# Performance work log

Hardware: AMD Instinct MI355X
Metric: run time of the kernel (lower is better)

The kernel has to match this reference:

```python
import jax, jax.numpy as jnp
import numpy as np

N_LIT, N_CLAUSE, N_EDGES, D = 100000, 400000, 1200000, 128


def setup_inputs() -> dict:
    key = jax.random.key(0)
    ks = jax.random.split(key, 9)
    s = 1.0 / np.sqrt(D)  # PyTorch LSTM init: U(-1/sqrt(hidden), 1/sqrt(hidden))
    x_l = jax.random.normal(ks[0], (N_LIT, D), jnp.float32)
    h0 = jax.random.normal(ks[1], (N_CLAUSE, D), jnp.float32)
    c0 = jax.random.normal(ks[2], (N_CLAUSE, D), jnp.float32)
    W_ih = jax.random.uniform(ks[3], (4 * D, D), jnp.float32, -s, s)
    W_hh = jax.random.uniform(ks[4], (4 * D, D), jnp.float32, -s, s)
    b_ih = jax.random.uniform(ks[5], (4 * D,), jnp.float32, -s, s)
    b_hh = jax.random.uniform(ks[6], (4 * D,), jnp.float32, -s, s)
    edge_lit = jax.random.randint(ks[7], (N_EDGES,), 0, N_LIT, jnp.int32)
    edge_clause = jnp.sort(jax.random.randint(ks[8], (N_EDGES,), 0, N_CLAUSE, jnp.int32))
    return {"x_l": x_l, "h0": h0, "c0": c0, "W_ih": W_ih, "W_hh": W_hh,
            "b_ih": b_ih, "b_hh": b_hh, "edge_lit": edge_lit, "edge_clause": edge_clause}


def reference(x_l, h0, c0, W_ih, W_hh, b_ih, b_hh, edge_lit, edge_clause):
    n_clauses = h0.shape[0]
    # msg = adj_t @ x_l : sparse aggregation of literal features into clauses
    msg = jax.ops.segment_sum(x_l[edge_lit], edge_clause, num_segments=n_clauses)  # [n_clauses, D]
    # Single-timestep LSTM cell (seq_len=1, batch=n_clauses); PyTorch gate order i,f,g,o
    gates = msg @ W_ih.T + b_ih + h0 @ W_hh.T + b_hh  # [n_clauses, 4D]
    i, f, g, o = jnp.split(gates, 4, axis=-1)
    i = jax.nn.sigmoid(i)
    f = jax.nn.sigmoid(f)
    g = jnp.tanh(g)
    o = jax.nn.sigmoid(o)
    c_new = f * c0 + i * g
    h_new = o * jnp.tanh(c_new)
    return (h_new, c_new)
```

## Files before the change

### kernel.cpp

```cpp
#include <hip/hip_runtime.h>
#include <hip/hip_bf16.h>


using frag_ab = __attribute__((ext_vector_type(8))) short;
using frag_cd = __attribute__((ext_vector_type(4))) float;

__device__ __forceinline__ float bf2f(unsigned short u) {
    union { unsigned u; float f; } v; v.u = ((unsigned)u) << 16; return v.f;
}
__device__ __forceinline__ unsigned short f2bf(float f) {
    __hip_bfloat16 h = __float2bfloat16(f);
    return *reinterpret_cast<unsigned short*>(&h);
}
__device__ __forceinline__ float sigm(float x) {
    return __builtin_amdgcn_rcpf(1.0f + __builtin_amdgcn_exp2f(-1.442695040889f * x));
}
__device__ __forceinline__ float tanh_fast(float x) {
    float s = __builtin_amdgcn_rcpf(1.0f + __builtin_amdgcn_exp2f(-2.885390081777f * x));
    return __builtin_fmaf(2.0f, s, -1.0f);
}
__device__ __forceinline__ frag_ab load8_fp32(const float* p) {
    float4 a = *reinterpret_cast<const float4*>(p);
    float4 b = *reinterpret_cast<const float4*>(p + 4);
    frag_ab r;
    r[0] = (short)f2bf(a.x); r[1] = (short)f2bf(a.y);
    r[2] = (short)f2bf(a.z); r[3] = (short)f2bf(a.w);
    r[4] = (short)f2bf(b.x); r[5] = (short)f2bf(b.y);
    r[6] = (short)f2bf(b.z); r[7] = (short)f2bf(b.w);
    return r;
}

#define WS_BPACK_OFF  0
#define WS_BIAS_OFF   262144
#define WS_FLAG_OFF   264192
#define WS_ROWPTR_OFF 264704

#define EDGE_CAP 512

__global__ void detect_fmt(const unsigned short* __restrict__ x, int* __restrict__ flag) {
    int t = threadIdx.x;
    int cnt = 0;
    for (int i = t; i < 4096; i += 64) {
        unsigned e = (x[2 * i] >> 7) & 0xFF;
        cnt += (e >= 0xC0) ? 1 : 0;
    }
    #pragma unroll
    for (int s = 32; s; s >>= 1) cnt += __shfl_xor(cnt, s);
    if (t == 0) *flag = (cnt > 64) ? 1 : 0;
}

__global__ void build_rowptr(const int* __restrict__ edge_clause, int* __restrict__ rowptr,
                             int n_edges, int n_clause) {
    int idx = blockIdx.x * blockDim.x + threadIdx.x;
    if (idx > n_clause) return;
    int lo = 0, hi = n_edges;
    while (lo < hi) {
        int mid = (lo + hi) >> 1;
        if (edge_clause[mid] < idx) lo = mid + 1; else hi = mid;
    }
    rowptr[idx] = lo;
}

template <int FP32IN>
__global__ void prepack(const void* __restrict__ W_ih_, const void* __restrict__ W_hh_,
                        const void* __restrict__ b_ih_, const void* __restrict__ b_hh_,
                        unsigned short* __restrict__ Bpack, float* __restrict__ bias,
                        const int* __restrict__ flag) {
    if (*flag != FP32IN) return;
    int idx = blockIdx.x * blockDim.x + threadIdx.x;
    if (idx < 16384) {
        int kk = idx >> 11;
        int n  = (idx >> 2) & 511;
        int lq = idx & 3;
        int ksrc = (kk & 3) * 32 + lq * 8;
        frag_ab v;
        if constexpr (FP32IN) {
            const float* W = (kk < 4) ? (const float*)W_ih_ : (const float*)W_hh_;
            v = load8_fp32(W + (size_t)n * 128 + ksrc);
        } else {
            const unsigned short* W =
                (kk < 4) ? (const unsigned short*)W_ih_ : (const unsigned short*)W_hh_;
            v = *reinterpret_cast<const frag_ab*>(W + (size_t)n * 128 + ksrc);
        }
        *reinterpret_cast<frag_ab*>(Bpack + (size_t)idx * 8) = v;
    }
    if (idx < 512) {
        float b;
        if constexpr (FP32IN)
            b = ((const float*)b_ih_)[idx] + ((const float*)b_hh_)[idx];
        else
            b = bf2f(((const unsigned short*)b_ih_)[idx]) +
                bf2f(((const unsigned short*)b_hh_)[idx]);
        bias[idx] = b;
    }
}

template <int FP32IN>
__global__ __launch_bounds__(512, 4) void lit2clause_fused(
    const void* __restrict__ x_l_,
    const void* __restrict__ h0_,
    const void* __restrict__ c0_,
    const unsigned short* __restrict__ Bpack,
    const float* __restrict__ bias,
    const int*  __restrict__ rowptr_g,
    const int*  __restrict__ edge_lit,
    void* __restrict__ out_,
    const int* __restrict__ fmt_flag,
    int n_clause)
{
    if (*fmt_flag != FP32IN) return;

    __shared__ __align__(16) unsigned char SH[32768];
    __shared__ int elits[EDGE_CAP];
    unsigned char* Amsg = SH;
    unsigned char* Ah0  = SH + 16384;
    float* LDSf = (float*)SH;

    const int tid  = threadIdx.x;
    const int lane = tid & 63;
    const int w    = tid >> 6;
    const int cbase = blockIdx.x * 64;

    int rp_l = 0;
    if (lane < 9) rp_l = rowptr_g[cbase + w * 8 + lane];

    const int eBase = rowptr_g[cbase];
    const int eEnd  = rowptr_g[cbase + 64];
    const int eCount = eEnd - eBase;
    for (int i = tid; i < eCount && i < EDGE_CAP; i += 512)
        elits[i] = edge_lit[eBase + i];

    #pragma unroll
    for (int q0 = 0; q0 < 2; ++q0) {
        int q = tid + q0 * 512;
        int row = q >> 4;
        int j   = q & 15;
        frag_ab v;
        if constexpr (FP32IN) {
            v = load8_fp32((const float*)h0_ + (size_t)(cbase + row) * 128 + j * 8);
        } else {
            v = *reinterpret_cast<const frag_ab*>(
                (const unsigned short*)h0_ + (size_t)(cbase + row) * 128 + j * 8);
        }
        int byte = (j * 16) ^ ((row & 7) << 4);
        *reinterpret_cast<frag_ab*>(Ah0 + row * 256 + byte) = v;
    }
    __syncthreads();

    {
        const int q   = lane >> 4;
        const int l16 = lane & 15;
        for (int s = 0; s < 8; ++s) {
            int cc = w * 8 + s;
            int st = __shfl(rp_l, s)     - eBase;
            int en = __shfl(rp_l, s + 1) - eBase;
            float a[8] = {0.f, 0.f, 0.f, 0.f, 0.f, 0.f, 0.f, 0.f};
            for (int e = st + q; e < en; e += 4) {
                int lit = (e < EDGE_CAP) ? elits[e] : edge_lit[eBase + e];
                if constexpr (FP32IN) {
                    const float* xr = (const float*)x_l_ + (size_t)lit * 128 + l16 * 8;
                    float4 v0 = *reinterpret_cast<const float4*>(xr);
                    float4 v1 = *reinterpret_cast<const float4*>(xr + 4);
                    a[0] += v0.x; a[1] += v0.y; a[2] += v0.z; a[3] += v0.w;
                    a[4] += v1.x; a[5] += v1.y; a[6] += v1.z; a[7] += v1.w;
                } else {
                    const unsigned short* xr =
                        (const unsigned short*)x_l_ + (size_t)lit * 128 + l16 * 8;
                    frag_ab v = *reinterpret_cast<const frag_ab*>(xr);
                    #pragma unroll
                    for (int j = 0; j < 8; ++j) a[j] += bf2f((unsigned short)v[j]);
                }
            }
            #pragma unroll
            for (int j = 0; j < 8; ++j) {
                a[j] += __shfl_xor(a[j], 16);
                a[j] += __shfl_xor(a[j], 32);
            }
            if (q == 0) {
                frag_ab o;
                #pragma unroll
                for (int j = 0; j < 8; ++j) o[j] = (short)f2bf(a[j]);
                int byte = (l16 * 16) ^ ((cc & 7) << 4);
                *reinterpret_cast<frag_ab*>(Amsg + cc * 256 + byte) = o;
            }
        }
    }
    __syncthreads();

    const int l15 = lane & 15;
    const int lq  = lane >> 4;
    const int d = w * 16 + l15;

    float cold[4][4];
    #pragma unroll
    for (int mf = 0; mf < 4; ++mf) {
        #pragma unroll
        for (int r = 0; r < 4; ++r) {
            int m = cbase + mf * 16 + lq * 4 + r;
            if constexpr (FP32IN) cold[mf][r] = ((const float*)c0_)[(size_t)m * 128 + d];
            else cold[mf][r] = bf2f(((const unsigned short*)c0_)[(size_t)m * 128 + d]);
        }
    }

    frag_cd acc[4][4];
    #pragma unroll
    for (int g = 0; g < 4; ++g)
        #pragma unroll
        for (int mf = 0; mf < 4; ++mf)
            acc[g][mf] = (frag_cd){0.f, 0.f, 0.f, 0.f};

    const frag_ab* Bp = reinterpret_cast<const frag_ab*>(Bpack);
    float bi[4];
    #pragma unroll
    for (int g = 0; g < 4; ++g) bi[g] = bias[g * 128 + d];

    #pragma unroll
    for (int kk = 0; kk < 8; ++kk) {
        const unsigned char* At = (kk < 4) ? Amsg : Ah0;
        frag_ab afr[4];
        #pragma unroll
        for (int mf = 0; mf < 4; ++mf) {
            int row = mf * 16 + l15;
            int byte = ((kk & 3) * 64 + lq * 16) ^ ((row & 7) << 4);
            afr[mf] = *reinterpret_cast<const frag_ab*>(At + row * 256 + byte);
        }
        frag_ab bfr[4];
        #pragma unroll
        for (int g = 0; g < 4; ++g) {
            int n = g * 128 + w * 16 + l15;
            bfr[g] = Bp[(kk * 512 + n) * 4 + lq];
        }
        #pragma unroll
        for (int g = 0; g < 4; ++g)
            #pragma unroll
            for (int mf = 0; mf < 4; ++mf)
                acc[g][mf] = __builtin_amdgcn_mfma_f32_16x16x32_bf16(
                    afr[mf], bfr[g], acc[g][mf], 0, 0, 0);
    }

    #pragma unroll
    for (int mf = 0; mf < 4; ++mf) {
        #pragma unroll
        for (int r = 0; r < 4; ++r) {
            float gi = acc[0][mf][r] + bi[0];
            float gf = acc[1][mf][r] + bi[1];
            float gg = acc[2][mf][r] + bi[2];
            float go = acc[3][mf][r] + bi[3];
            float iv = sigm(gi);
            float fv = sigm(gf);
            float gv = tanh_fast(gg);
            float ov = sigm(go);
            float cn = fv * cold[mf][r] + iv * gv;
            float hn = ov * tanh_fast(cn);
            acc[0][mf][r] = hn;
            acc[1][mf][r] = cn;
        }
    }

    #pragma unroll
    for (int half = 0; half < 2; ++half) {
        __syncthreads();
        #pragma unroll
        for (int mf = 0; mf < 4; ++mf) {
            #pragma unroll
            for (int r = 0; r < 4; ++r) {
                int rl = mf * 16 + lq * 4 + r;
                int idx = rl * 128 + ((((d >> 2) ^ (rl & 7)) << 2) | (d & 3));
                LDSf[idx] = acc[half][mf][r];
            }
        }
        __syncthreads();
        if constexpr (FP32IN) {
            float* outp = (float*)out_ + (size_t)half * n_clause * 128;
            #pragma unroll
            for (int q0 = 0; q0 < 4; ++q0) {
                int q = tid + q0 * 512;
                int row = q >> 5;
                int j   = q & 31;
                float4 v = *reinterpret_cast<const float4*>(
                    &LDSf[row * 128 + ((j ^ (row & 7)) << 2)]);
                *reinterpret_cast<float4*>(outp + (size_t)(cbase + row) * 128 + j * 4) = v;
            }
        } else {
            unsigned short* outp = (unsigned short*)out_ + (size_t)half * n_clause * 128;
            #pragma unroll
            for (int q0 = 0; q0 < 2; ++q0) {
                int q = tid + q0 * 512;
                int row = q >> 4;
                int jj  = q & 15;
                int j0 = 2 * jj, j1 = 2 * jj + 1;
                float4 f0 = *reinterpret_cast<const float4*>(
                    &LDSf[row * 128 + ((j0 ^ (row & 7)) << 2)]);
                float4 f1 = *reinterpret_cast<const float4*>(
                    &LDSf[row * 128 + ((j1 ^ (row & 7)) << 2)]);
                frag_ab o;
                o[0] = (short)f2bf(f0.x); o[1] = (short)f2bf(f0.y);
                o[2] = (short)f2bf(f0.z); o[3] = (short)f2bf(f0.w);
                o[4] = (short)f2bf(f1.x); o[5] = (short)f2bf(f1.y);
                o[6] = (short)f2bf(f1.z); o[7] = (short)f2bf(f1.w);
                *reinterpret_cast<frag_ab*>(outp + (size_t)(cbase + row) * 128 + jj * 8) = o;
            }
        }
    }
}

extern "C" void kernel_launch(void* const* d_in, const int* in_sizes, int n_in,
                              void* d_out, int out_size, void* d_ws, size_t ws_size,
                              hipStream_t stream) {
    const void* x_l  = d_in[0];
    const void* h0   = d_in[1];
    const void* c0   = d_in[2];
    const void* W_ih = d_in[3];
    const void* W_hh = d_in[4];
    const void* b_ih = d_in[5];
    const void* b_hh = d_in[6];
    const int* edge_lit    = (const int*)d_in[7];
    const int* edge_clause = (const int*)d_in[8];

    int n_edges  = in_sizes[7];
    int n_clause = in_sizes[1] / 128;
    int nblocks  = (n_clause + 63) / 64;

    unsigned char* ws = (unsigned char*)d_ws;
    unsigned short* Bpack = (unsigned short*)(ws + WS_BPACK_OFF);
    float* bias  = (float*)(ws + WS_BIAS_OFF);
    int* flag    = (int*)(ws + WS_FLAG_OFF);
    int* rowptr  = (int*)(ws + WS_ROWPTR_OFF);

    detect_fmt<<<1, 64, 0, stream>>>((const unsigned short*)x_l, flag);

    build_rowptr<<<(n_clause + 256) / 256, 256, 0, stream>>>(
        edge_clause, rowptr, n_edges, n_clause);

    prepack<1><<<64, 256, 0, stream>>>(W_ih, W_hh, b_ih, b_hh, Bpack, bias, flag);
    prepack<0><<<64, 256, 0, stream>>>(W_ih, W_hh, b_ih, b_hh, Bpack, bias, flag);

    lit2clause_fused<1><<<nblocks, 512, 0, stream>>>(
        x_l, h0, c0, Bpack, bias, rowptr, edge_lit, d_out, flag, n_clause);
    lit2clause_fused<0><<<nblocks, 512, 0, stream>>>(
        x_l, h0, c0, Bpack, bias, rowptr, edge_lit, d_out, flag, n_clause);
}
```

Measured before the change: 346.2 us.

## Make fused LSTM kernel persistent with next-tile prefetch and transposed MFMA outputs

Converts the fused gather+LSTM kernel into a persistent grid of at most 512 blocks that loops over 64-clause tiles. While the current tile is aggregated, each block prefetches the next tile's row pointers, edge literals and h0 rows into registers. It also swaps the MFMA operands so each lane holds 4 consecutive features, enabling float4 loads of c0 and bias and vectorized LDS stores. The edge staging now covers only the first 512 edges per tile in LDS, and fewer resident blocks may reduce latency hiding for the gathers.

```diff
diff --git a/kernel.cpp b/kernel.cpp
--- a/kernel.cpp
+++ b/kernel.cpp
@@ -119,186 +119,210 @@
     const int tid  = threadIdx.x;
     const int lane = tid & 63;
     const int w    = tid >> 6;
-    const int cbase = blockIdx.x * 64;
-
-    int rp_l = 0;
-    if (lane < 9) rp_l = rowptr_g[cbase + w * 8 + lane];
-
-    const int eBase = rowptr_g[cbase];
-    const int eEnd  = rowptr_g[cbase + 64];
-    const int eCount = eEnd - eBase;
-    for (int i = tid; i < eCount && i < EDGE_CAP; i += 512)
-        elits[i] = edge_lit[eBase + i];
-
-    #pragma unroll
-    for (int q0 = 0; q0 < 2; ++q0) {
-        int q = tid + q0 * 512;
-        int row = q >> 4;
-        int j   = q & 15;
-        frag_ab v;
+    const int l15  = lane & 15;
+    const int lq   = lane >> 4;
+    const int ntiles = (n_clause + 63) >> 6;
+
+    frag_ab h0s0, h0s1;
+    int elit_s = 0, rp_s = 0, eB_s = 0, eE_s = 0;
+
+    auto stage_tile = [&](int tile) {
+        int cb = tile * 64;
+        rp_s = (lane < 9) ? rowptr_g[cb + w * 8 + lane] : 0;
+        eB_s = rowptr_g[cb];
+        eE_s = rowptr_g[cb + 64];
+        int cnt = eE_s - eB_s;
+        elit_s = (tid < cnt) ? edge_lit[eB_s + tid] : 0;
+        int q0r = tid >> 4, q0j = tid & 15;
+        int q1r = (tid + 512) >> 4, q1j = tid & 15;
         if constexpr (FP32IN) {
-            v = load8_fp32((const float*)h0_ + (size_t)(cbase + row) * 128 + j * 8);
+            h0s0 = load8_fp32((const float*)h0_ + (size_t)(cb + q0r) * 128 + q0j * 8);
+            h0s1 = load8_fp32((const float*)h0_ + (size_t)(cb + q1r) * 128 + q1j * 8);
         } else {
-            v = *reinterpret_cast<const frag_ab*>(
-                (const unsigned short*)h0_ + (size_t)(cbase + row) * 128 + j * 8);
-        }
-        int byte = (j * 16) ^ ((row & 7) << 4);
-        *reinterpret_cast<frag_ab*>(Ah0 + row * 256 + byte) = v;
-    }
-    __syncthreads();
-
-    {
-        const int q   = lane >> 4;
-        const int l16 = lane & 15;
-        for (int s = 0; s < 8; ++s) {
-            int cc = w * 8 + s;
-            int st = __shfl(rp_l, s)     - eBase;
-            int en = __shfl(rp_l, s + 1) - eBase;
-            float a[8] = {0.f, 0.f, 0.f, 0.f, 0.f, 0.f, 0.f, 0.f};
-            for (int e = st + q; e < en; e += 4) {
-                int lit = (e < EDGE_CAP) ? elits[e] : edge_lit[eBase + e];
-                if constexpr (FP32IN) {
-                    const float* xr = (const float*)x_l_ + (size_t)lit * 128 + l16 * 8;
-                    float4 v0 = *reinterpret_cast<const float4*>(xr);
-                    float4 v1 = *reinterpret_cast<const float4*>(xr + 4);
-                    a[0] += v0.x; a[1] += v0.y; a[2] += v0.z; a[3] += v0.w;
-                    a[4] += v1.x; a[5] += v1.y; a[6] += v1.z; a[7] += v1.w;
-                } else {
-                    const unsigned short* xr =
-                        (const unsigned short*)x_l_ + (size_t)lit * 128 + l16 * 8;
-                    frag_ab v = *reinterpret_cast<const frag_ab*>(xr);
+            h0s0 = *reinterpret_cast<const frag_ab*>(
+                (const unsigned short*)h0_ + (size_t)(cb + q0r) * 128 + q0j * 8);
+            h0s1 = *reinterpret_cast<const frag_ab*>(
+                (const unsigned short*)h0_ + (size_t)(cb + q1r) * 128 + q1j * 8);
+        }
+    };
+
+    int tb = blockIdx.x;
+    if (tb >= ntiles) return;
+    stage_tile(tb);
+
+    for (; tb < ntiles; tb += gridDim.x) {
+        const int cbase = tb * 64;
+        const int rp_l  = rp_s;
+        const int eBase = eB_s;
+        const int eCnt  = eE_s - eB_s;
+
+        __syncthreads();
+        {
+            int row0 = tid >> 4, j = tid & 15;
+            *reinterpret_cast<frag_ab*>(
+                Ah0 + row0 * 256 + ((j * 16) ^ ((row0 & 7) << 4))) = h0s0;
+            int row1 = (tid + 512) >> 4;
+            *reinterpret_cast<frag_ab*>(
+                Ah0 + row1 * 256 + ((j * 16) ^ ((row1 & 7) << 4))) = h0s1;
+            if (tid < eCnt) elits[tid] = elit_s;
+        }
+        __syncthreads();
+
+        {
+            const int q = lane >> 4;
+            for (int s = 0; s < 8; ++s) {
+                int cc = w * 8 + s;
+                int st = __shfl(rp_l, s)     - eBase;
+                int en = __shfl(rp_l, s + 1) - eBase;
+                float a[8] = {0.f, 0.f, 0.f, 0.f, 0.f, 0.f, 0.f, 0.f};
+                for (int e = st + q; e < en; e += 4) {
+                    int lit = (e < EDGE_CAP) ? elits[e] : edge_lit[eBase + e];
+                    if constexpr (FP32IN) {
+                        const float* xr = (const float*)x_l_ + (size_t)lit * 128 + l15 * 8;
+                        float4 v0 = *reinterpret_cast<const float4*>(xr);
+                        float4 v1 = *reinterpret_cast<const float4*>(xr + 4);
+                        a[0] += v0.x; a[1] += v0.y; a[2] += v0.z; a[3] += v0.w;
+                        a[4] += v1.x; a[5] += v1.y; a[6] += v1.z; a[7] += v1.w;
+                    } else {
+                        const unsigned short* xr =
+                            (const unsigned short*)x_l_ + (size_t)lit * 128 + l15 * 8;
+                        frag_ab v = *reinterpret_cast<const frag_ab*>(xr);
+                        #pragma unroll
+                        for (int j = 0; j < 8; ++j) a[j] += bf2f((unsigned short)v[j]);
+                    }
+                }
+                #pragma unroll
+                for (int j = 0; j < 8; ++j) {
+                    a[j] += __shfl_xor(a[j], 16);
+                    a[j] += __shfl_xor(a[j], 32);
+                }
+                if (q == 0) {
+                    frag_ab o;
                     #pragma unroll
-                    for (int j = 0; j < 8; ++j) a[j] += bf2f((unsigned short)v[j]);
-                }
-            }
-            #pragma unroll
-            for (int j = 0; j < 8; ++j) {
-                a[j] += __shfl_xor(a[j], 16);
-                a[j] += __shfl_xor(a[j], 32);
-            }
-            if (q == 0) {
-                frag_ab o;
+                    for (int j = 0; j < 8; ++j) o[j] = (short)f2bf(a[j]);
+                    *reinterpret_cast<frag_ab*>(
+                        Amsg + cc * 256 + ((l15 * 16) ^ ((cc & 7) << 4))) = o;
+                }
+            }
+        }
+        {
+            int tn = tb + gridDim.x;
+            if (tn >= ntiles) tn = tb;
+            stage_tile(tn);
+        }
+        __syncthreads();
+
+        frag_cd acc[4][4];
+        #pragma unroll
+        for (int g = 0; g < 4; ++g)
+            #pragma unroll
+            for (int mf = 0; mf < 4; ++mf)
+                acc[g][mf] = (frag_cd){0.f, 0.f, 0.f, 0.f};
+
+        const frag_ab* Bp = reinterpret_cast<const frag_ab*>(Bpack);
+        #pragma unroll
+        for (int kk = 0; kk < 8; ++kk) {
+            const unsigned char* At = (kk < 4) ? Amsg : Ah0;
+            frag_ab afr[4];
+            #pragma unroll
+            for (int mf = 0; mf < 4; ++mf) {
+                int row = mf * 16 + l15;
+                int byte = ((kk & 3) * 64 + lq * 16) ^ ((row & 7) << 4);
+                afr[mf] = *reinterpret_cast<const frag_ab*>(At + row * 256 + byte);
+            }
+            frag_ab bfr[4];
+            #pragma unroll
+            for (int g = 0; g < 4; ++g) {
+                int n = g * 128 + w * 16 + l15;
+                bfr[g] = Bp[(kk * 512 + n) * 4 + lq];
+            }
+            #pragma unroll
+            for (int g = 0; g < 4; ++g)
                 #pragma unroll
-                for (int j = 0; j < 8; ++j) o[j] = (short)f2bf(a[j]);
-                int byte = (l16 * 16) ^ ((cc & 7) << 4);
-                *reinterpret_cast<frag_ab*>(Amsg + cc * 256 + byte) = o;
-            }
-        }
-    }
-    __syncthreads();
-
-    const int l15 = lane & 15;
-    const int lq  = lane >> 4;
-    const int d = w * 16 + l15;
-
-    float cold[4][4];
-    #pragma unroll
-    for (int mf = 0; mf < 4; ++mf) {
-        #pragma unroll
-        for (int r = 0; r < 4; ++r) {
-            int m = cbase + mf * 16 + lq * 4 + r;
-            if constexpr (FP32IN) cold[mf][r] = ((const float*)c0_)[(size_t)m * 128 + d];
-            else cold[mf][r] = bf2f(((const unsigned short*)c0_)[(size_t)m * 128 + d]);
-        }
-    }
-
-    frag_cd acc[4][4];
-    #pragma unroll
-    for (int g = 0; g < 4; ++g)
-        #pragma unroll
-        for (int mf = 0; mf < 4; ++mf)
-            acc[g][mf] = (frag_cd){0.f, 0.f, 0.f, 0.f};
-
-    const frag_ab* Bp = reinterpret_cast<const frag_ab*>(Bpack);
-    float bi[4];
-    #pragma unroll
-    for (int g = 0; g < 4; ++g) bi[g] = bias[g * 128 + d];
-
-    #pragma unroll
-    for (int kk = 0; kk < 8; ++kk) {
-        const unsigned char* At = (kk < 4) ? Amsg : Ah0;
-        frag_ab afr[4];
+                for (int mf = 0; mf < 4; ++mf)
+                    acc[g][mf] = __builtin_amdgcn_mfma_f32_16x16x32_bf16(
+                        bfr[g], afr[mf], acc[g][mf], 0, 0, 0);
+        }
+
+        const int d0 = w * 16 + lq * 4;
+        float4 bv[4];
+        #pragma unroll
+        for (int g = 0; g < 4; ++g)
+            bv[g] = *reinterpret_cast<const float4*>(bias + g * 128 + d0);
+
         #pragma unroll
         for (int mf = 0; mf < 4; ++mf) {
-            int row = mf * 16 + l15;
-            int byte = ((kk & 3) * 64 + lq * 16) ^ ((row & 7) << 4);
-            afr[mf] = *reinterpret_cast<const frag_ab*>(At + row * 256 + byte);
-        }
-        frag_ab bfr[4];
-        #pragma unroll
-        for (int g = 0; g < 4; ++g) {
-            int n = g * 128 + w * 16 + l15;
-            bfr[g] = Bp[(kk * 512 + n) * 4 + lq];
-        }
-        #pragma unroll
-        for (int g = 0; g < 4; ++g)
-            #pragma unroll
-            for (int mf = 0; mf < 4; ++mf)
-                acc[g][mf] = __builtin_amdgcn_mfma_f32_16x16x32_bf16(
-                    afr[mf], bfr[g], acc[g][mf], 0, 0, 0);
-    }
-
-    #pragma unroll
-    for (int mf = 0; mf < 4; ++mf) {
-        #pragma unroll
-        for (int r = 0; r < 4; ++r) {
-            float gi = acc[0][mf][r] + bi[0];
-            float gf = acc[1][mf][r] + bi[1];
-            float gg = acc[2][mf][r] + bi[2];
-            float go = acc[3][mf][r] + bi[3];
-            float iv = sigm(gi);
-            float fv = sigm(gf);
-            float gv = tanh_fast(gg);
-            float ov = sigm(go);
-            float cn = fv * cold[mf][r] + iv * gv;
-            float hn = ov * tanh_fast(cn);
-            acc[0][mf][r] = hn;
-            acc[1][mf][r] = cn;
-        }
-    }
-
-    #pragma unroll
-    for (int half = 0; half < 2; ++half) {
-        __syncthreads();
-        #pragma unroll
-        for (int mf = 0; mf < 4; ++mf) {
+            int m = cbase + mf * 16 + l15;
+            float cva[4];
+            if constexpr (FP32IN) {
+                float4 cv = *reinterpret_cast<const float4*>(
+                    (const float*)c0_ + (size_t)m * 128 + d0);
+                cva[0] = cv.x; cva[1] = cv.y; cva[2] = cv.z; cva[3] = cv.w;
+            } else {
+                ushort4 cu = *reinterpret_cast<const ushort4*>(
+                    (const unsigned short*)c0_ + (size_t)m * 128 + d0);
+                cva[0] = bf2f(cu.x); cva[1] = bf2f(cu.y);
+                cva[2] = bf2f(cu.z); cva[3] = bf2f(cu.w);
+            }
             #pragma unroll
             for (int r = 0; r < 4; ++r) {
-                int rl = mf * 16 + lq * 4 + r;
-                int idx = rl * 128 + ((((d >> 2) ^ (rl & 7)) << 2) | (d & 3));
-                LDSf[idx] = acc[half][mf][r];
-            }
-        }
-        __syncthreads();
-        if constexpr (FP32IN) {
-            float* outp = (float*)out_ + (size_t)half * n_clause * 128;
-            #pragma unroll
-            for (int q0 = 0; q0 < 4; ++q0) {
-                int q = tid + q0 * 512;
-                int row = q >> 5;
-                int j   = q & 31;
-                float4 v = *reinterpret_cast<const float4*>(
-                    &LDSf[row * 128 + ((j ^ (row & 7)) << 2)]);
-                *reinterpret_cast<float4*>(outp + (size_t)(cbase + row) * 128 + j * 4) = v;
-            }
-        } else {
-            unsigned short* outp = (unsigned short*)out_ + (size_t)half * n_clause * 128;
-            #pragma unroll
-            for (int q0 = 0; q0 < 2; ++q0) {
-                int q = tid + q0 * 512;
-                int row = q >> 4;
-                int jj  = q & 15;
-                int j0 = 2 * jj, j1 = 2 * jj + 1;
-                float4 f0 = *reinterpret_cast<const float4*>(
-                    &LDSf[row * 128 + ((j0 ^ (row & 7)) << 2)]);
-                float4 f1 = *reinterpret_cast<const float4*>(
-                    &LDSf[row * 128 + ((j1 ^ (row & 7)) << 2)]);
-                frag_ab o;
-                o[0] = (short)f2bf(f0.x); o[1] = (short)f2bf(f0.y);
-                o[2] = (short)f2bf(f0.z); o[3] = (short)f2bf(f0.w);
-                o[4] = (short)f2bf(f1.x); o[5] = (short)f2bf(f1.y);
-                o[6] = (short)f2bf(f1.z); o[7] = (short)f2bf(f1.w);
-                *reinterpret_cast<frag_ab*>(outp + (size_t)(cbase + row) * 128 + jj * 8) = o;
+                float gi = acc[0][mf][r] + bv[0][r];
+                float gf = acc[1][mf][r] + bv[1][r];
+                float gg = acc[2][mf][r] + bv[2][r];
+                float go = acc[3][mf][r] + bv[3][r];
+                float iv = sigm(gi);
+                float fv = sigm(gf);
+                float gv = tanh_fast(gg);
+                float ov = sigm(go);
+                float cn = fv * cva[r] + iv * gv;
+                float hn = ov * tanh_fast(cn);
+                acc[0][mf][r] = hn;
+                acc[1][mf][r] = cn;
+            }
+        }
+
+        #pragma unroll
+        for (int half = 0; half < 2; ++half) {
+            __syncthreads();
+            #pragma unroll
+            for (int mf = 0; mf < 4; ++mf) {
+                int rl = mf * 16 + l15;
+                int cch = (w * 4 + lq) ^ (rl & 7);
+                *reinterpret_cast<frag_cd*>(&LDSf[rl * 128 + cch * 4]) = acc[half][mf];
+            }
+            __syncthreads();
+            if constexpr (FP32IN) {
+                float* outp = (float*)out_ + (size_t)half * n_clause * 128;
+                #pragma unroll
+                for (int q0 = 0; q0 < 4; ++q0) {
+                    int q = tid + q0 * 512;
+                    int row = q >> 5;
+                    int j   = q & 31;
+                    float4 v = *reinterpret_cast<const float4*>(
+                        &LDSf[row * 128 + ((j ^ (row & 7)) << 2)]);
+                    *reinterpret_cast<float4*>(
+                        outp + (size_t)(cbase + row) * 128 + j * 4) = v;
+                }
+            } else {
+                unsigned short* outp = (unsigned short*)out_ + (size_t)half * n_clause * 128;
+                #pragma unroll
+                for (int q0 = 0; q0 < 2; ++q0) {
+                    int q = tid + q0 * 512;
+                    int row = q >> 4;
+                    int jj  = q & 15;
+                    int j0 = 2 * jj, j1 = 2 * jj + 1;
+                    float4 f0 = *reinterpret_cast<const float4*>(
+                        &LDSf[row * 128 + ((j0 ^ (row & 7)) << 2)]);
+                    float4 f1 = *reinterpret_cast<const float4*>(
+                        &LDSf[row * 128 + ((j1 ^ (row & 7)) << 2)]);
+                    frag_ab o;
+                    o[0] = (short)f2bf(f0.x); o[1] = (short)f2bf(f0.y);
+                    o[2] = (short)f2bf(f0.z); o[3] = (short)f2bf(f0.w);
+                    o[4] = (short)f2bf(f1.x); o[5] = (short)f2bf(f1.y);
+                    o[6] = (short)f2bf(f1.z); o[7] = (short)f2bf(f1.w);
+                    *reinterpret_cast<frag_ab*>(
+                        outp + (size_t)(cbase + row) * 128 + jj * 8) = o;
+                }
             }
         }
     }
@@ -319,7 +343,8 @@
 
     int n_edges  = in_sizes[7];
     int n_clause = in_sizes[1] / 128;
-    int nblocks  = (n_clause + 63) / 64;
+    int ntiles   = (n_clause + 63) / 64;
+    int nblocks  = ntiles < 512 ? ntiles : 512;
 
     unsigned char* ws = (unsigned char*)d_ws;
     unsigned short* Bpack = (unsigned short*)(ws + WS_BPACK_OFF);
```

Result: slower. 967.1 us (+179.3%).
